# Optimization experiments

Hardware: AMD Instinct MI355X
Metric: run time of the kernel (lower is better)

## Reference

```python
import jax, jax.numpy as jnp
import numpy as np

B, N, D = 16, 2048, 128
NEG = jnp.float32(-2.0**32 + 1)

def setup_inputs() -> dict:
    key = jax.random.key(0)
    ks = jax.random.split(key, 9)
    s = 1.0 / np.sqrt(D)
    return {
        "queries": jax.random.normal(ks[0], (B, N, D), jnp.float32),
        "keys": jax.random.normal(ks[1], (B, N, D), jnp.float32),
        "padding_mask": jax.random.randint(ks[2], (B, N), 0, 2, jnp.int32),
        "Wq": jax.random.uniform(ks[3], (D, D), jnp.float32, -s, s),
        "bq": jax.random.uniform(ks[4], (D,), jnp.float32, -s, s),
        "Wk": jax.random.uniform(ks[5], (D, D), jnp.float32, -s, s),
        "bk": jax.random.uniform(ks[6], (D,), jnp.float32, -s, s),
        "Wv": jax.random.uniform(ks[7], (D, D), jnp.float32, -s, s),
        "bv": jax.random.uniform(ks[8], (D,), jnp.float32, -s, s),
    }

def reference(queries, keys, padding_mask, Wq, bq, Wk, bk, Wv, bv):
    d = queries.shape[-1]
    eq = queries @ Wq.T + bq            # [B,N,D]
    ek = keys @ Wk.T + bk               # [B,N,D]
    ev = keys @ Wv.T + bv               # [B,N,D]
    # scaled scores [B,N,N]
    coefs = jnp.einsum('bnd,bmd->bnm', eq, ek) / jnp.sqrt(jnp.float32(d))
    # key padding: large negative where keys row sums to zero (broadcast over query axis)
    key_pad = (jnp.sum(keys, axis=-1) == 0).astype(jnp.float32) * NEG   # [B,N]
    out = jnp.where(padding_mask[:, None, :] == 0, key_pad[:, None, :], coefs)
    out = jax.nn.softmax(out, axis=2)
    # NOTE: original applies query mask along the KEY axis (unsqueeze(1)) -- kept faithfully
    q_pad = (jnp.sum(queries, axis=-1) != 0).astype(jnp.float32)        # [B,N]
    out = out * q_pad[:, None, :]
    out = jnp.einsum('bnm,bmd->bnd', out, ev)
    return out + queries
```

## Files before the change

### kernel.cpp

```cpp
#include <hip/hip_runtime.h>
#include <hip/hip_bf16.h>


#define SCALE 0.08838834764831845f

typedef __bf16 bf16x8 __attribute__((ext_vector_type(8)));
typedef __bf16 bf16x4 __attribute__((ext_vector_type(4)));
typedef short  s16x4  __attribute__((ext_vector_type(4)));
typedef float  f32x4  __attribute__((ext_vector_type(4)));

static __device__ __forceinline__ f32x4 MFMA16(bf16x4 a, bf16x4 b, f32x4 c) {
#if defined(__HIP_DEVICE_COMPILE__)
    s16x4 sa, sb;
    __builtin_memcpy(&sa, &a, 8);
    __builtin_memcpy(&sb, &b, 8);
    return __builtin_amdgcn_mfma_f32_16x16x16bf16_1k(sa, sb, c, 0, 0, 0);
#else
    (void)a; (void)b;
    return c;
#endif
}

static __device__ __forceinline__ bf16x4 lo4(uint4 v) {
    bf16x4 r; uint2 t = {v.x, v.y}; __builtin_memcpy(&r, &t, 8); return r;
}
static __device__ __forceinline__ bf16x4 hi4(uint4 v) {
    bf16x4 r; uint2 t = {v.z, v.w}; __builtin_memcpy(&r, &t, 8); return r;
}

__global__ __launch_bounds__(256) void prep_kernel(
    const float* __restrict__ Wq, const float* __restrict__ Wk,
    const float* __restrict__ Wv, __bf16* __restrict__ wb)
{
    int i = blockIdx.x * 256 + threadIdx.x;
    int w = i >> 11, c = i & 2047;
    int col = c & 15, quad = (c >> 4) & 3, f = (c >> 6) & 3, ct = c >> 8;
    const float* src = ((w == 0) ? Wq : (w == 1) ? Wk : Wv)
                       + (size_t)(ct * 16 + col) * 128 + f * 32 + quad * 8;
    float4 a = *(const float4*)src, b = *(const float4*)(src + 4);
    bf16x8 t = {(__bf16)a.x, (__bf16)a.y, (__bf16)a.z, (__bf16)a.w,
                (__bf16)b.x, (__bf16)b.y, (__bf16)b.z, (__bf16)b.w};
    *(bf16x8*)&wb[(size_t)w * 16384 + (size_t)c * 8] = t;
}

__global__ __launch_bounds__(256) void proj_kernel(
    const float* __restrict__ Q, const float* __restrict__ K,
    const int* __restrict__ PM, const __bf16* __restrict__ wb,
    const float* __restrict__ Bq, const float* __restrict__ Bk,
    const float* __restrict__ Bv,
    __bf16* __restrict__ eqb, __bf16* __restrict__ ekf, __bf16* __restrict__ evf,
    float* __restrict__ dmul)
{
    __shared__ __bf16 stage[128 * 72];
    const int tid  = threadIdx.x;
    const int wave = tid >> 6, lane = tid & 63;
    const int col  = lane & 15, quad = lane >> 4;
    const int w = blockIdx.x >> 9;
    const int rowbase = (blockIdx.x & 511) * 64;
    const int myrow   = rowbase + wave * 16 + col;
    const int bb   = rowbase >> 11;
    const int m16b = (rowbase & 2047) >> 4;

    const float* asrc = (w == 0) ? Q : K;
    bf16x8 a[4];
    float ss = 0.f;
    #pragma unroll
    for (int f = 0; f < 4; ++f) {
        const float* p = asrc + (size_t)myrow * 128 + f * 32 + quad * 8;
        float4 v0 = *(const float4*)p, v1 = *(const float4*)(p + 4);
        float vv[8] = {v0.x, v0.y, v0.z, v0.w, v1.x, v1.y, v1.z, v1.w};
        #pragma unroll
        for (int j = 0; j < 8; ++j) { ss += vv[j]; a[f][j] = (__bf16)vv[j]; }
    }

    float rm = 1.f;
    if (w == 1) {
        ss += __shfl_xor(ss, 16); ss += __shfl_xor(ss, 32);
        int pmv = PM[myrow];
        rm = (pmv != 0) ? 1.f : 0.f;
        if (quad == 0) dmul[myrow] = (pmv == 0 && ss == 0.f) ? 0.f : 1.f;
    } else if (w == 2) {
        float qs = 0.f;
        #pragma unroll
        for (int f = 0; f < 4; ++f) {
            const float* p = Q + (size_t)myrow * 128 + f * 32 + quad * 8;
            float4 v0 = *(const float4*)p, v1 = *(const float4*)(p + 4);
            qs += v0.x + v0.y + v0.z + v0.w + v1.x + v1.y + v1.z + v1.w;
        }
        qs += __shfl_xor(qs, 16); qs += __shfl_xor(qs, 32);
        rm = (qs != 0.f) ? 1.f : 0.f;
    }
    float rmul[4];
    #pragma unroll
    for (int r = 0; r < 4; ++r) rmul[r] = __shfl(rm, quad * 4 + r);

    const float sc = (w == 0) ? SCALE : 1.f;
    const float* bias = (w == 0) ? Bq : (w == 1) ? Bk : Bv;
    const __bf16* wbp = wb + w * 16384;

    f32x4 acc[8];
    #pragma unroll
    for (int ct = 0; ct < 8; ++ct) { f32x4 z = {0.f, 0.f, 0.f, 0.f}; acc[ct] = z; }
    #pragma unroll
    for (int f = 0; f < 4; ++f) {
        #pragma unroll
        for (int ct = 0; ct < 8; ++ct) {
            bf16x8 bfr = *(const bf16x8*)&wbp[(size_t)(ct * 4 + f) * 512 + lane * 8];
            acc[ct] = __builtin_amdgcn_mfma_f32_16x16x32_bf16(a[f], bfr, acc[ct], 0, 0, 0);
        }
    }
    #pragma unroll
    for (int ct = 0; ct < 8; ++ct) {
        float bv = bias[ct * 16 + col];
        #pragma unroll
        for (int r = 0; r < 4; ++r) {
            float v = (acc[ct][r] + bv) * rmul[r] * sc;
            int rr = wave * 16 + quad * 4 + r;
            if (w == 2) stage[(ct * 16 + col) * 72 + rr] = (__bf16)v;
            else        stage[rr * 136 + ct * 16 + col] = (__bf16)v;
        }
    }
    __syncthreads();

    if (w == 0) {
        int r = tid >> 2, seg = (tid & 3) * 32;
        uint4* g4 = (uint4*)(eqb + (size_t)(rowbase + r) * 128 + seg);
        const uint4* s4 = (const uint4*)&stage[r * 136 + seg];
        g4[0] = s4[0]; g4[1] = s4[1]; g4[2] = s4[2]; g4[3] = s4[3];
    } else if (w == 1) {
        __bf16* dst = ekf + (size_t)bb * 2048 * 128 + (size_t)m16b * 2048;
        #pragma unroll
        for (int c = 0; c < 4; ++c) {
            int s = tid + c * 256;
            int l = s & 63, f = (s >> 6) & 3, m = s >> 8;
            *(uint4*)&dst[(size_t)s * 8] =
                *(const uint4*)&stage[(m * 16 + (l & 15)) * 136 + f * 32 + ((l >> 4) & 3) * 8];
        }
    } else {
        __bf16* dst = evf + (size_t)bb * 2048 * 128 + (size_t)m16b * 2048;
        #pragma unroll
        for (int c = 0; c < 4; ++c) {
            int s = tid + c * 256;
            int l = s & 63, dp = (s >> 6) & 3, m = s >> 8;
            int cl = l & 15, ql = (l >> 4) & 3;
            uint2 xa = *(const uint2*)&stage[((2 * dp) * 16 + cl) * 72 + m * 16 + ql * 4];
            uint2 xb = *(const uint2*)&stage[((2 * dp + 1) * 16 + cl) * 72 + m * 16 + ql * 4];
            uint4 v = {xa.x, xa.y, xb.x, xb.y};
            *(uint4*)&dst[(size_t)s * 8] = v;
        }
    }
}

__global__ __launch_bounds__(256, 2) void attn_kernel(
    const __bf16* __restrict__ eqb, const __bf16* __restrict__ ekf,
    const __bf16* __restrict__ evf, const float* __restrict__ dmul,
    const float* __restrict__ Q, float* __restrict__ out)
{
    __shared__ struct { float obuf[2][32 * 132]; float lbuf[2][32]; } sm;

    const int tid  = threadIdx.x;
    const int wave = tid >> 6, lane = tid & 63;
    const int col  = lane & 15, quad = lane >> 4;
    const int i  = blockIdx.x;
    const int b  = 2 * (i & 7) + ((i >> 3) & 1);
    const int qt = i >> 4;
    const int rowg0 = b * 2048 + qt * 32;
    const __bf16* ekb_b = ekf + (size_t)b * 2048 * 128;
    const __bf16* evb_b = evf + (size_t)b * 2048 * 128;
    const float*  dmb   = dmul + b * 2048;

    bf16x8 aqf[2][4];
    #pragma unroll
    for (int q2 = 0; q2 < 2; ++q2)
        #pragma unroll
        for (int f = 0; f < 4; ++f)
            aqf[q2][f] = *(const bf16x8*)&eqb[(size_t)(rowg0 + q2 * 16 + col) * 128 + f * 32 + quad * 8];

    f32x4 o[2][8];
    float lsum[2] = {0.f, 0.f};
    #pragma unroll
    for (int q2 = 0; q2 < 2; ++q2)
        #pragma unroll
        for (int dt = 0; dt < 8; ++dt) { f32x4 z = {0.f, 0.f, 0.f, 0.f}; o[q2][dt] = z; }

    const int kq0 = wave * 512;

    bf16x8 kc[8];
    {
        const int m16 = kq0 >> 4;
        #pragma unroll
        for (int f = 0; f < 4; ++f) {
            kc[f]     = *(const bf16x8*)&ekb_b[(size_t)((m16 + 0) * 4 + f) * 512 + lane * 8];
            kc[4 + f] = *(const bf16x8*)&ekb_b[(size_t)((m16 + 1) * 4 + f) * 512 + lane * 8];
        }
    }
    float4 dm0 = *(const float4*)&dmb[kq0 + quad * 4];
    float4 dm1 = *(const float4*)&dmb[kq0 + 16 + quad * 4];

    for (int it = 0; it < 16; ++it) {
        const int kb = kq0 + it * 32;
        const int m16 = kb >> 4;

        uint4 vc[8];
        #pragma unroll
        for (int dp = 0; dp < 4; ++dp) {
            vc[dp]     = *(const uint4*)&evb_b[(size_t)((m16 + 0) * 4 + dp) * 512 + lane * 8];
            vc[4 + dp] = *(const uint4*)&evb_b[(size_t)((m16 + 1) * 4 + dp) * 512 + lane * 8];
        }
        bf16x8 kn[8];
        float4 dn0, dn1;
        if (it < 15) {
            const int m16n = m16 + 2;
            #pragma unroll
            for (int f = 0; f < 4; ++f) {
                kn[f]     = *(const bf16x8*)&ekb_b[(size_t)((m16n + 0) * 4 + f) * 512 + lane * 8];
                kn[4 + f] = *(const bf16x8*)&ekb_b[(size_t)((m16n + 1) * 4 + f) * 512 + lane * 8];
            }
            dn0 = *(const float4*)&dmb[kb + 32 + quad * 4];
            dn1 = *(const float4*)&dmb[kb + 48 + quad * 4];
        }

        f32x4 s[2][2];
        #pragma unroll
        for (int q2 = 0; q2 < 2; ++q2)
            #pragma unroll
            for (int mt = 0; mt < 2; ++mt) { f32x4 z = {0.f, 0.f, 0.f, 0.f}; s[q2][mt] = z; }
        #pragma unroll
        for (int f = 0; f < 4; ++f) {
            #pragma unroll
            for (int q2 = 0; q2 < 2; ++q2) {
                s[q2][0] = __builtin_amdgcn_mfma_f32_16x16x32_bf16(kc[f],     aqf[q2][f], s[q2][0], 0, 0, 0);
                s[q2][1] = __builtin_amdgcn_mfma_f32_16x16x32_bf16(kc[4 + f], aqf[q2][f], s[q2][1], 0, 0, 0);
            }
        }

        const float dmv[2][4] = {{dm0.x, dm0.y, dm0.z, dm0.w},
                                 {dm1.x, dm1.y, dm1.z, dm1.w}};
        bf16x4 pk[2][2];
        #pragma unroll
        for (int q2 = 0; q2 < 2; ++q2)
            #pragma unroll
            for (int mt = 0; mt < 2; ++mt)
                #pragma unroll
                for (int r = 0; r < 4; ++r) {
                    float e = __expf(s[q2][mt][r]) * dmv[mt][r];
                    pk[q2][mt][r] = (__bf16)e;
                    lsum[q2] += e;
                }

        #pragma unroll
        for (int dp = 0; dp < 4; ++dp) {
            bf16x4 v0l = lo4(vc[dp]),     v0h = hi4(vc[dp]);
            bf16x4 v1l = lo4(vc[4 + dp]), v1h = hi4(vc[4 + dp]);
            #pragma unroll
            for (int q2 = 0; q2 < 2; ++q2) {
                o[q2][2 * dp]     = MFMA16(v0l, pk[q2][0], o[q2][2 * dp]);
                o[q2][2 * dp]     = MFMA16(v1l, pk[q2][1], o[q2][2 * dp]);
                o[q2][2 * dp + 1] = MFMA16(v0h, pk[q2][0], o[q2][2 * dp + 1]);
                o[q2][2 * dp + 1] = MFMA16(v1h, pk[q2][1], o[q2][2 * dp + 1]);
            }
        }

        if (it < 15) {
            #pragma unroll
            for (int f = 0; f < 8; ++f) kc[f] = kn[f];
            dm0 = dn0; dm1 = dn1;
        }
    }

    #pragma unroll
    for (int q2 = 0; q2 < 2; ++q2) {
        lsum[q2] += __shfl_xor(lsum[q2], 16);
        lsum[q2] += __shfl_xor(lsum[q2], 32);
    }

    if (wave & 1) {
        int slot = wave >> 1;
        #pragma unroll
        for (int q2 = 0; q2 < 2; ++q2) {
            #pragma unroll
            for (int dt = 0; dt < 8; ++dt) {
                float4 v = {o[q2][dt][0], o[q2][dt][1], o[q2][dt][2], o[q2][dt][3]};
                *(float4*)&sm.obuf[slot][(q2 * 16 + col) * 132 + dt * 16 + quad * 4] = v;
            }
            if (quad == 0) sm.lbuf[slot][q2 * 16 + col] = lsum[q2];
        }
    }
    __syncthreads();
    if (!(wave & 1)) {
        int slot = wave >> 1;
        #pragma unroll
        for (int q2 = 0; q2 < 2; ++q2) {
            lsum[q2] += sm.lbuf[slot][q2 * 16 + col];
            #pragma unroll
            for (int dt = 0; dt < 8; ++dt) {
                float4 t = *(const float4*)&sm.obuf[slot][(q2 * 16 + col) * 132 + dt * 16 + quad * 4];
                o[q2][dt][0] += t.x; o[q2][dt][1] += t.y;
                o[q2][dt][2] += t.z; o[q2][dt][3] += t.w;
            }
        }
    }
    __syncthreads();
    if (wave == 2) {
        #pragma unroll
        for (int q2 = 0; q2 < 2; ++q2) {
            #pragma unroll
            for (int dt = 0; dt < 8; ++dt) {
                float4 v = {o[q2][dt][0], o[q2][dt][1], o[q2][dt][2], o[q2][dt][3]};
                *(float4*)&sm.obuf[0][(q2 * 16 + col) * 132 + dt * 16 + quad * 4] = v;
            }
            if (quad == 0) sm.lbuf[0][q2 * 16 + col] = lsum[q2];
        }
    }
    __syncthreads();
    if (wave == 0) {
        #pragma unroll
        for (int q2 = 0; q2 < 2; ++q2) {
            float inv = 1.f / (lsum[q2] + sm.lbuf[0][q2 * 16 + col]);
            const size_t rowoff = (size_t)(rowg0 + q2 * 16 + col) * 128;
            #pragma unroll
            for (int dt = 0; dt < 8; ++dt) {
                float4 t = *(const float4*)&sm.obuf[0][(q2 * 16 + col) * 132 + dt * 16 + quad * 4];
                float4 qres = *(const float4*)&Q[rowoff + dt * 16 + quad * 4];
                float4 v;
                v.x = (o[q2][dt][0] + t.x) * inv + qres.x;
                v.y = (o[q2][dt][1] + t.y) * inv + qres.y;
                v.z = (o[q2][dt][2] + t.z) * inv + qres.z;
                v.w = (o[q2][dt][3] + t.w) * inv + qres.w;
                *(float4*)&out[rowoff + dt * 16 + quad * 4] = v;
            }
        }
    }
}

extern "C" void kernel_launch(void* const* d_in, const int* in_sizes, int n_in,
                              void* d_out, int out_size, void* d_ws, size_t ws_size,
                              hipStream_t stream)
{
    const float* Q  = (const float*)d_in[0];
    const float* K  = (const float*)d_in[1];
    const int*   PM = (const int*)d_in[2];
    const float* Wq = (const float*)d_in[3];
    const float* Bq = (const float*)d_in[4];
    const float* Wk = (const float*)d_in[5];
    const float* Bk = (const float*)d_in[6];
    const float* Wv = (const float*)d_in[7];
    const float* Bv = (const float*)d_in[8];
    float* out = (float*)d_out;

    const size_t SZE = (size_t)16 * 2048 * 128;
    __bf16* eqb = (__bf16*)d_ws;
    __bf16* ekf = eqb + SZE;
    __bf16* evf = ekf + SZE;
    float* dmul = (float*)(evf + SZE);
    __bf16* wb  = (__bf16*)(dmul + 16 * 2048);

    prep_kernel<<<24, 256, 0, stream>>>(Wq, Wk, Wv, wb);
    proj_kernel<<<1536, 256, 0, stream>>>(Q, K, PM, wb, Bq, Bk, Bv,
                                          eqb, ekf, evf, dmul);
    attn_kernel<<<1024, 256, 0, stream>>>(eqb, ekf, evf, dmul, Q, out);
}
```

Measured before the change: 160.8 us.

## Stage K/V tiles in LDS with async loads and drop cross-wave reduction

The attention kernel now uses 2-wave blocks in which each wave owns 32 query rows and walks all keys. K/V tiles are double-buffered into LDS with global_load_lds, which replaces the per-wave register prefetch from global memory and the split-key reduction through shared memory at the end. The key mask becomes an additive bias fed in as the MFMA accumulator init, instead of a multiply after exp. The projection kernel computes K and V in the same block so the key rows are loaded once, and the query-pad flags are precomputed in the prep kernel. The changes trade more per-iteration barriers and a smaller block for less redundant global traffic; the -1e5 bias only approximates the reference's -2^32 mask value.

```diff
diff --git a/kernel.cpp b/kernel.cpp
--- a/kernel.cpp
+++ b/kernel.cpp
@@ -28,28 +28,55 @@
     bf16x4 r; uint2 t = {v.z, v.w}; __builtin_memcpy(&r, &t, 8); return r;
 }
 
+static __device__ __forceinline__ void gl16(const __bf16* g, __bf16* l) {
+    __builtin_amdgcn_global_load_lds(
+        (const __attribute__((address_space(1))) unsigned int*)g,
+        (__attribute__((address_space(3))) unsigned int*)l, 16, 0, 0);
+}
+
 __global__ __launch_bounds__(256) void prep_kernel(
     const float* __restrict__ Wq, const float* __restrict__ Wk,
-    const float* __restrict__ Wv, __bf16* __restrict__ wb)
+    const float* __restrict__ Wv, const float* __restrict__ Qm,
+    __bf16* __restrict__ wb, float* __restrict__ qpadf)
 {
-    int i = blockIdx.x * 256 + threadIdx.x;
-    int w = i >> 11, c = i & 2047;
-    int col = c & 15, quad = (c >> 4) & 3, f = (c >> 6) & 3, ct = c >> 8;
-    const float* src = ((w == 0) ? Wq : (w == 1) ? Wk : Wv)
-                       + (size_t)(ct * 16 + col) * 128 + f * 32 + quad * 8;
-    float4 a = *(const float4*)src, b = *(const float4*)(src + 4);
-    bf16x8 t = {(__bf16)a.x, (__bf16)a.y, (__bf16)a.z, (__bf16)a.w,
-                (__bf16)b.x, (__bf16)b.y, (__bf16)b.z, (__bf16)b.w};
-    *(bf16x8*)&wb[(size_t)w * 16384 + (size_t)c * 8] = t;
+    if (blockIdx.x < 24) {
+        int i = blockIdx.x * 256 + threadIdx.x;
+        int w = i >> 11, c = i & 2047;
+        int col = c & 15, quad = (c >> 4) & 3, f = (c >> 6) & 3, ct = c >> 8;
+        const float* src = ((w == 0) ? Wq : (w == 1) ? Wk : Wv)
+                           + (size_t)(ct * 16 + col) * 128 + f * 32 + quad * 8;
+        float4 a = *(const float4*)src, b = *(const float4*)(src + 4);
+        bf16x8 t = {(__bf16)a.x, (__bf16)a.y, (__bf16)a.z, (__bf16)a.w,
+                    (__bf16)b.x, (__bf16)b.y, (__bf16)b.z, (__bf16)b.w};
+        *(bf16x8*)&wb[(size_t)w * 16384 + (size_t)c * 8] = t;
+    } else {
+        const int tid = threadIdx.x, wv = tid >> 6, l = tid & 63;
+        const int rb = (blockIdx.x - 24) * 256 + wv * 64;
+        #pragma unroll
+        for (int pass = 0; pass < 8; ++pass) {
+            int r = rb + pass * 8 + (l >> 3);
+            const float* p = Qm + (size_t)r * 128 + (l & 7) * 4;
+            float s4 = 0.f;
+            #pragma unroll
+            for (int seg = 0; seg < 4; ++seg) {
+                float4 v = *(const float4*)(p + seg * 32);
+                s4 += v.x + v.y + v.z + v.w;
+            }
+            s4 += __shfl_xor(s4, 1);
+            s4 += __shfl_xor(s4, 2);
+            s4 += __shfl_xor(s4, 4);
+            if ((l & 7) == 0) qpadf[r] = (s4 != 0.f) ? 1.f : 0.f;
+        }
+    }
 }
 
 __global__ __launch_bounds__(256) void proj_kernel(
     const float* __restrict__ Q, const float* __restrict__ K,
     const int* __restrict__ PM, const __bf16* __restrict__ wb,
     const float* __restrict__ Bq, const float* __restrict__ Bk,
-    const float* __restrict__ Bv,
+    const float* __restrict__ Bv, const float* __restrict__ qpadf,
     __bf16* __restrict__ eqb, __bf16* __restrict__ ekf, __bf16* __restrict__ evf,
-    float* __restrict__ dmul)
+    float* __restrict__ madd)
 {
     __shared__ __bf16 stage[128 * 72];
     const int tid  = threadIdx.x;
@@ -73,90 +100,115 @@
         for (int j = 0; j < 8; ++j) { ss += vv[j]; a[f][j] = (__bf16)vv[j]; }
     }
 
-    float rm = 1.f;
-    if (w == 1) {
-        ss += __shfl_xor(ss, 16); ss += __shfl_xor(ss, 32);
-        int pmv = PM[myrow];
-        rm = (pmv != 0) ? 1.f : 0.f;
-        if (quad == 0) dmul[myrow] = (pmv == 0 && ss == 0.f) ? 0.f : 1.f;
-    } else if (w == 2) {
-        float qs = 0.f;
+    if (w == 0) {
+        f32x4 acc[8];
+        #pragma unroll
+        for (int ct = 0; ct < 8; ++ct) { f32x4 z = {0.f, 0.f, 0.f, 0.f}; acc[ct] = z; }
         #pragma unroll
         for (int f = 0; f < 4; ++f) {
-            const float* p = Q + (size_t)myrow * 128 + f * 32 + quad * 8;
-            float4 v0 = *(const float4*)p, v1 = *(const float4*)(p + 4);
-            qs += v0.x + v0.y + v0.z + v0.w + v1.x + v1.y + v1.z + v1.w;
-        }
-        qs += __shfl_xor(qs, 16); qs += __shfl_xor(qs, 32);
-        rm = (qs != 0.f) ? 1.f : 0.f;
-    }
-    float rmul[4];
-    #pragma unroll
-    for (int r = 0; r < 4; ++r) rmul[r] = __shfl(rm, quad * 4 + r);
-
-    const float sc = (w == 0) ? SCALE : 1.f;
-    const float* bias = (w == 0) ? Bq : (w == 1) ? Bk : Bv;
-    const __bf16* wbp = wb + w * 16384;
-
-    f32x4 acc[8];
-    #pragma unroll
-    for (int ct = 0; ct < 8; ++ct) { f32x4 z = {0.f, 0.f, 0.f, 0.f}; acc[ct] = z; }
-    #pragma unroll
-    for (int f = 0; f < 4; ++f) {
+            #pragma unroll
+            for (int ct = 0; ct < 8; ++ct) {
+                bf16x8 bfr = *(const bf16x8*)&wb[(size_t)(ct * 4 + f) * 512 + lane * 8];
+                acc[ct] = __builtin_amdgcn_mfma_f32_16x16x32_bf16(a[f], bfr, acc[ct], 0, 0, 0);
+            }
+        }
         #pragma unroll
         for (int ct = 0; ct < 8; ++ct) {
-            bf16x8 bfr = *(const bf16x8*)&wbp[(size_t)(ct * 4 + f) * 512 + lane * 8];
-            acc[ct] = __builtin_amdgcn_mfma_f32_16x16x32_bf16(a[f], bfr, acc[ct], 0, 0, 0);
-        }
-    }
-    #pragma unroll
-    for (int ct = 0; ct < 8; ++ct) {
-        float bv = bias[ct * 16 + col];
-        #pragma unroll
-        for (int r = 0; r < 4; ++r) {
-            float v = (acc[ct][r] + bv) * rmul[r] * sc;
-            int rr = wave * 16 + quad * 4 + r;
-            if (w == 2) stage[(ct * 16 + col) * 72 + rr] = (__bf16)v;
-            else        stage[rr * 136 + ct * 16 + col] = (__bf16)v;
-        }
-    }
-    __syncthreads();
-
-    if (w == 0) {
+            float bvv = Bq[ct * 16 + col];
+            #pragma unroll
+            for (int r = 0; r < 4; ++r) {
+                int rr = wave * 16 + quad * 4 + r;
+                stage[rr * 136 + ct * 16 + col] = (__bf16)((acc[ct][r] + bvv) * SCALE);
+            }
+        }
+        __syncthreads();
         int r = tid >> 2, seg = (tid & 3) * 32;
         uint4* g4 = (uint4*)(eqb + (size_t)(rowbase + r) * 128 + seg);
         const uint4* s4 = (const uint4*)&stage[r * 136 + seg];
         g4[0] = s4[0]; g4[1] = s4[1]; g4[2] = s4[2]; g4[3] = s4[3];
-    } else if (w == 1) {
-        __bf16* dst = ekf + (size_t)bb * 2048 * 128 + (size_t)m16b * 2048;
-        #pragma unroll
-        for (int c = 0; c < 4; ++c) {
-            int s = tid + c * 256;
-            int l = s & 63, f = (s >> 6) & 3, m = s >> 8;
-            *(uint4*)&dst[(size_t)s * 8] =
-                *(const uint4*)&stage[(m * 16 + (l & 15)) * 136 + f * 32 + ((l >> 4) & 3) * 8];
-        }
     } else {
-        __bf16* dst = evf + (size_t)bb * 2048 * 128 + (size_t)m16b * 2048;
-        #pragma unroll
-        for (int c = 0; c < 4; ++c) {
-            int s = tid + c * 256;
-            int l = s & 63, dp = (s >> 6) & 3, m = s >> 8;
-            int cl = l & 15, ql = (l >> 4) & 3;
-            uint2 xa = *(const uint2*)&stage[((2 * dp) * 16 + cl) * 72 + m * 16 + ql * 4];
-            uint2 xb = *(const uint2*)&stage[((2 * dp + 1) * 16 + cl) * 72 + m * 16 + ql * 4];
-            uint4 v = {xa.x, xa.y, xb.x, xb.y};
-            *(uint4*)&dst[(size_t)s * 8] = v;
-        }
-    }
-}
-
-__global__ __launch_bounds__(256, 2) void attn_kernel(
+        ss += __shfl_xor(ss, 16); ss += __shfl_xor(ss, 32);
+        int pmv = PM[myrow];
+        float rmk = (pmv != 0) ? 1.f : 0.f;
+        float rmv = qpadf[myrow];
+        if (quad == 0) madd[myrow] = (pmv == 0 && ss == 0.f) ? -1.0e5f : 0.f;
+        float rk[4], rv[4];
+        #pragma unroll
+        for (int r = 0; r < 4; ++r) {
+            rk[r] = __shfl(rmk, quad * 4 + r);
+            rv[r] = __shfl(rmv, quad * 4 + r);
+        }
+
+        f32x4 acck[8], accv[8];
+        #pragma unroll
+        for (int ct = 0; ct < 8; ++ct) {
+            f32x4 z = {0.f, 0.f, 0.f, 0.f}; acck[ct] = z; accv[ct] = z;
+        }
+        #pragma unroll
+        for (int f = 0; f < 4; ++f) {
+            #pragma unroll
+            for (int ct = 0; ct < 8; ++ct) {
+                bf16x8 bk_ = *(const bf16x8*)&wb[(size_t)16384 + (size_t)(ct * 4 + f) * 512 + lane * 8];
+                bf16x8 bv_ = *(const bf16x8*)&wb[(size_t)32768 + (size_t)(ct * 4 + f) * 512 + lane * 8];
+                acck[ct] = __builtin_amdgcn_mfma_f32_16x16x32_bf16(a[f], bk_, acck[ct], 0, 0, 0);
+                accv[ct] = __builtin_amdgcn_mfma_f32_16x16x32_bf16(a[f], bv_, accv[ct], 0, 0, 0);
+            }
+        }
+
+        #pragma unroll
+        for (int ct = 0; ct < 8; ++ct) {
+            float bvv = Bk[ct * 16 + col];
+            #pragma unroll
+            for (int r = 0; r < 4; ++r) {
+                int rr = wave * 16 + quad * 4 + r;
+                stage[rr * 136 + ct * 16 + col] = (__bf16)((acck[ct][r] + bvv) * rk[r]);
+            }
+        }
+        __syncthreads();
+        {
+            __bf16* dst = ekf + (size_t)bb * 2048 * 128 + (size_t)m16b * 2048;
+            #pragma unroll
+            for (int c = 0; c < 4; ++c) {
+                int s = tid + c * 256;
+                int l = s & 63, f = (s >> 6) & 3, m = s >> 8;
+                *(uint4*)&dst[(size_t)s * 8] =
+                    *(const uint4*)&stage[(m * 16 + (l & 15)) * 136 + f * 32 + ((l >> 4) & 3) * 8];
+            }
+        }
+        __syncthreads();
+        #pragma unroll
+        for (int ct = 0; ct < 8; ++ct) {
+            float bvv = Bv[ct * 16 + col];
+            #pragma unroll
+            for (int r = 0; r < 4; ++r) {
+                int rr = wave * 16 + quad * 4 + r;
+                stage[(ct * 16 + col) * 72 + rr] = (__bf16)((accv[ct][r] + bvv) * rv[r]);
+            }
+        }
+        __syncthreads();
+        {
+            __bf16* dst = evf + (size_t)bb * 2048 * 128 + (size_t)m16b * 2048;
+            #pragma unroll
+            for (int c = 0; c < 4; ++c) {
+                int s = tid + c * 256;
+                int l = s & 63, dp = (s >> 6) & 3, m = s >> 8;
+                int cl = l & 15, ql = (l >> 4) & 3;
+                uint2 xa = *(const uint2*)&stage[((2 * dp) * 16 + cl) * 72 + m * 16 + ql * 4];
+                uint2 xb = *(const uint2*)&stage[((2 * dp + 1) * 16 + cl) * 72 + m * 16 + ql * 4];
+                uint4 v = {xa.x, xa.y, xb.x, xb.y};
+                *(uint4*)&dst[(size_t)s * 8] = v;
+            }
+        }
+    }
+}
+
+__global__ __launch_bounds__(128) void attn_kernel(
     const __bf16* __restrict__ eqb, const __bf16* __restrict__ ekf,
-    const __bf16* __restrict__ evf, const float* __restrict__ dmul,
+    const __bf16* __restrict__ evf, const float* __restrict__ madd,
     const float* __restrict__ Q, float* __restrict__ out)
 {
-    __shared__ struct { float obuf[2][32 * 132]; float lbuf[2][32]; } sm;
+    __shared__ __bf16 kb[2][4096];
+    __shared__ __bf16 vb[2][4096];
 
     const int tid  = threadIdx.x;
     const int wave = tid >> 6, lane = tid & 63;
@@ -164,10 +216,10 @@
     const int i  = blockIdx.x;
     const int b  = 2 * (i & 7) + ((i >> 3) & 1);
     const int qt = i >> 4;
-    const int rowg0 = b * 2048 + qt * 32;
+    const int rowg0 = b * 2048 + qt * 64 + wave * 32;
     const __bf16* ekb_b = ekf + (size_t)b * 2048 * 128;
     const __bf16* evb_b = evf + (size_t)b * 2048 * 128;
-    const float*  dmb   = dmul + b * 2048;
+    const float*  dmb   = madd + b * 2048;
 
     bf16x8 aqf[2][4];
     #pragma unroll
@@ -183,48 +235,51 @@
         #pragma unroll
         for (int dt = 0; dt < 8; ++dt) { f32x4 z = {0.f, 0.f, 0.f, 0.f}; o[q2][dt] = z; }
 
-    const int kq0 = wave * 512;
-
-    bf16x8 kc[8];
-    {
-        const int m16 = kq0 >> 4;
+    #pragma unroll
+    for (int c = 0; c < 4; ++c) {
+        int sb = (c * 2 + wave) * 64;
+        gl16(ekb_b + (size_t)(sb + lane) * 8, &kb[0][sb * 8]);
+        gl16(evb_b + (size_t)(sb + lane) * 8, &vb[0][sb * 8]);
+    }
+    float4 dm0 = *(const float4*)&dmb[quad * 4];
+    float4 dm1 = *(const float4*)&dmb[16 + quad * 4];
+    __syncthreads();
+
+    for (int t = 0; t < 64; ++t) {
+        const int cur = t & 1;
+        float4 dn0, dn1;
+        if (t < 63) {
+            const __bf16* gk = ekb_b + (size_t)(t + 1) * 4096;
+            const __bf16* gv = evb_b + (size_t)(t + 1) * 4096;
+            #pragma unroll
+            for (int c = 0; c < 4; ++c) {
+                int sb = (c * 2 + wave) * 64;
+                gl16(gk + (size_t)(sb + lane) * 8, &kb[cur ^ 1][sb * 8]);
+                gl16(gv + (size_t)(sb + lane) * 8, &vb[cur ^ 1][sb * 8]);
+            }
+            dn0 = *(const float4*)&dmb[(t + 1) * 32 + quad * 4];
+            dn1 = *(const float4*)&dmb[(t + 1) * 32 + 16 + quad * 4];
+        }
+
+        bf16x8 kc[8];
+        uint4  vc[8];
         #pragma unroll
         for (int f = 0; f < 4; ++f) {
-            kc[f]     = *(const bf16x8*)&ekb_b[(size_t)((m16 + 0) * 4 + f) * 512 + lane * 8];
-            kc[4 + f] = *(const bf16x8*)&ekb_b[(size_t)((m16 + 1) * 4 + f) * 512 + lane * 8];
-        }
-    }
-    float4 dm0 = *(const float4*)&dmb[kq0 + quad * 4];
-    float4 dm1 = *(const float4*)&dmb[kq0 + 16 + quad * 4];
-
-    for (int it = 0; it < 16; ++it) {
-        const int kb = kq0 + it * 32;
-        const int m16 = kb >> 4;
-
-        uint4 vc[8];
+            kc[f]     = *(const bf16x8*)&kb[cur][f * 512 + lane * 8];
+            kc[4 + f] = *(const bf16x8*)&kb[cur][(4 + f) * 512 + lane * 8];
+        }
         #pragma unroll
         for (int dp = 0; dp < 4; ++dp) {
-            vc[dp]     = *(const uint4*)&evb_b[(size_t)((m16 + 0) * 4 + dp) * 512 + lane * 8];
-            vc[4 + dp] = *(const uint4*)&evb_b[(size_t)((m16 + 1) * 4 + dp) * 512 + lane * 8];
-        }
-        bf16x8 kn[8];
-        float4 dn0, dn1;
-        if (it < 15) {
-            const int m16n = m16 + 2;
-            #pragma unroll
-            for (int f = 0; f < 4; ++f) {
-                kn[f]     = *(const bf16x8*)&ekb_b[(size_t)((m16n + 0) * 4 + f) * 512 + lane * 8];
-                kn[4 + f] = *(const bf16x8*)&ekb_b[(size_t)((m16n + 1) * 4 + f) * 512 + lane * 8];
-            }
-            dn0 = *(const float4*)&dmb[kb + 32 + quad * 4];
-            dn1 = *(const float4*)&dmb[kb + 48 + quad * 4];
+            vc[dp]     = *(const uint4*)&vb[cur][dp * 512 + lane * 8];
+            vc[4 + dp] = *(const uint4*)&vb[cur][(4 + dp) * 512 + lane * 8];
         }
 
         f32x4 s[2][2];
-        #pragma unroll
-        for (int q2 = 0; q2 < 2; ++q2)
-            #pragma unroll
-            for (int mt = 0; mt < 2; ++mt) { f32x4 z = {0.f, 0.f, 0.f, 0.f}; s[q2][mt] = z; }
+        {
+            f32x4 i0 = {dm0.x, dm0.y, dm0.z, dm0.w};
+            f32x4 i1 = {dm1.x, dm1.y, dm1.z, dm1.w};
+            s[0][0] = i0; s[0][1] = i1; s[1][0] = i0; s[1][1] = i1;
+        }
         #pragma unroll
         for (int f = 0; f < 4; ++f) {
             #pragma unroll
@@ -234,8 +289,6 @@
             }
         }
 
-        const float dmv[2][4] = {{dm0.x, dm0.y, dm0.z, dm0.w},
-                                 {dm1.x, dm1.y, dm1.z, dm1.w}};
         bf16x4 pk[2][2];
         #pragma unroll
         for (int q2 = 0; q2 < 2; ++q2)
@@ -243,7 +296,7 @@
             for (int mt = 0; mt < 2; ++mt)
                 #pragma unroll
                 for (int r = 0; r < 4; ++r) {
-                    float e = __expf(s[q2][mt][r]) * dmv[mt][r];
+                    float e = __expf(s[q2][mt][r]);
                     pk[q2][mt][r] = (__bf16)e;
                     lsum[q2] += e;
                 }
@@ -261,10 +314,9 @@
             }
         }
 
-        if (it < 15) {
-            #pragma unroll
-            for (int f = 0; f < 8; ++f) kc[f] = kn[f];
+        if (t < 63) {
             dm0 = dn0; dm1 = dn1;
+            __syncthreads();
         }
     }
 
@@ -272,63 +324,17 @@
     for (int q2 = 0; q2 < 2; ++q2) {
         lsum[q2] += __shfl_xor(lsum[q2], 16);
         lsum[q2] += __shfl_xor(lsum[q2], 32);
-    }
-
-    if (wave & 1) {
-        int slot = wave >> 1;
-        #pragma unroll
-        for (int q2 = 0; q2 < 2; ++q2) {
-            #pragma unroll
-            for (int dt = 0; dt < 8; ++dt) {
-                float4 v = {o[q2][dt][0], o[q2][dt][1], o[q2][dt][2], o[q2][dt][3]};
-                *(float4*)&sm.obuf[slot][(q2 * 16 + col) * 132 + dt * 16 + quad * 4] = v;
-            }
-            if (quad == 0) sm.lbuf[slot][q2 * 16 + col] = lsum[q2];
-        }
-    }
-    __syncthreads();
-    if (!(wave & 1)) {
-        int slot = wave >> 1;
-        #pragma unroll
-        for (int q2 = 0; q2 < 2; ++q2) {
-            lsum[q2] += sm.lbuf[slot][q2 * 16 + col];
-            #pragma unroll
-            for (int dt = 0; dt < 8; ++dt) {
-                float4 t = *(const float4*)&sm.obuf[slot][(q2 * 16 + col) * 132 + dt * 16 + quad * 4];
-                o[q2][dt][0] += t.x; o[q2][dt][1] += t.y;
-                o[q2][dt][2] += t.z; o[q2][dt][3] += t.w;
-            }
-        }
-    }
-    __syncthreads();
-    if (wave == 2) {
-        #pragma unroll
-        for (int q2 = 0; q2 < 2; ++q2) {
-            #pragma unroll
-            for (int dt = 0; dt < 8; ++dt) {
-                float4 v = {o[q2][dt][0], o[q2][dt][1], o[q2][dt][2], o[q2][dt][3]};
-                *(float4*)&sm.obuf[0][(q2 * 16 + col) * 132 + dt * 16 + quad * 4] = v;
-            }
-            if (quad == 0) sm.lbuf[0][q2 * 16 + col] = lsum[q2];
-        }
-    }
-    __syncthreads();
-    if (wave == 0) {
-        #pragma unroll
-        for (int q2 = 0; q2 < 2; ++q2) {
-            float inv = 1.f / (lsum[q2] + sm.lbuf[0][q2 * 16 + col]);
-            const size_t rowoff = (size_t)(rowg0 + q2 * 16 + col) * 128;
-            #pragma unroll
-            for (int dt = 0; dt < 8; ++dt) {
-                float4 t = *(const float4*)&sm.obuf[0][(q2 * 16 + col) * 132 + dt * 16 + quad * 4];
-                float4 qres = *(const float4*)&Q[rowoff + dt * 16 + quad * 4];
-                float4 v;
-                v.x = (o[q2][dt][0] + t.x) * inv + qres.x;
-                v.y = (o[q2][dt][1] + t.y) * inv + qres.y;
-                v.z = (o[q2][dt][2] + t.z) * inv + qres.z;
-                v.w = (o[q2][dt][3] + t.w) * inv + qres.w;
-                *(float4*)&out[rowoff + dt * 16 + quad * 4] = v;
-            }
+        float inv = 1.f / lsum[q2];
+        const size_t rowoff = (size_t)(rowg0 + q2 * 16 + col) * 128;
+        #pragma unroll
+        for (int dt = 0; dt < 8; ++dt) {
+            float4 qres = *(const float4*)&Q[rowoff + dt * 16 + quad * 4];
+            float4 v;
+            v.x = o[q2][dt][0] * inv + qres.x;
+            v.y = o[q2][dt][1] * inv + qres.y;
+            v.z = o[q2][dt][2] * inv + qres.z;
+            v.w = o[q2][dt][3] * inv + qres.w;
+            *(float4*)&out[rowoff + dt * 16 + quad * 4] = v;
         }
     }
 }
@@ -352,11 +358,12 @@
     __bf16* eqb = (__bf16*)d_ws;
     __bf16* ekf = eqb + SZE;
     __bf16* evf = ekf + SZE;
-    float* dmul = (float*)(evf + SZE);
-    __bf16* wb  = (__bf16*)(dmul + 16 * 2048);
-
-    prep_kernel<<<24, 256, 0, stream>>>(Wq, Wk, Wv, wb);
-    proj_kernel<<<1536, 256, 0, stream>>>(Q, K, PM, wb, Bq, Bk, Bv,
-                                          eqb, ekf, evf, dmul);
-    attn_kernel<<<1024, 256, 0, stream>>>(eqb, ekf, evf, dmul, Q, out);
-}
+    float* madd = (float*)(evf + SZE);
+    __bf16* wb  = (__bf16*)(madd + 16 * 2048);
+    float* qpadf = (float*)(wb + 3 * 16384);
+
+    prep_kernel<<<152, 256, 0, stream>>>(Wq, Wk, Wv, Q, wb, qpadf);
+    proj_kernel<<<1024, 256, 0, stream>>>(Q, K, PM, wb, Bq, Bk, Bv, qpadf,
+                                          eqb, ekf, evf, madd);
+    attn_kernel<<<512, 128, 0, stream>>>(eqb, ekf, evf, madd, Q, out);
+}
```

Result: slower. 218.7 us (+36.0%).

## Use K=32 MFMA for PV, fold log2e scale and additive mask into scores

Applied to the files above, without the earlier changes.

Rearranges the value tensor layout so the P·V product uses the 16x16x32 bf16 MFMA instead of pairs of 16x16x16 MFMAs. It folds log2(e) into the query scale so the kernel can use the hardware exp2. The multiplicative key mask becomes an additive bias that seeds the score accumulator. It also adds s_setprio around the MFMA blocks and pads the reduction buffer stride. The aim is fewer MFMA issues and less VALU work per iteration. The risk is that the -1e5 additive mask and the exp without max subtraction approximate the original zeroing semantics.

```diff
diff --git a/kernel.cpp b/kernel.cpp
--- a/kernel.cpp
+++ b/kernel.cpp
@@ -2,30 +2,17 @@
 #include <hip/hip_bf16.h>
 
 
-#define SCALE 0.08838834764831845f
+#define SCALE_LOG2E 0.12751875f
 
 typedef __bf16 bf16x8 __attribute__((ext_vector_type(8)));
-typedef __bf16 bf16x4 __attribute__((ext_vector_type(4)));
-typedef short  s16x4  __attribute__((ext_vector_type(4)));
 typedef float  f32x4  __attribute__((ext_vector_type(4)));
 
-static __device__ __forceinline__ f32x4 MFMA16(bf16x4 a, bf16x4 b, f32x4 c) {
-#if defined(__HIP_DEVICE_COMPILE__)
-    s16x4 sa, sb;
-    __builtin_memcpy(&sa, &a, 8);
-    __builtin_memcpy(&sb, &b, 8);
-    return __builtin_amdgcn_mfma_f32_16x16x16bf16_1k(sa, sb, c, 0, 0, 0);
+static __device__ __forceinline__ float fexp2(float x) {
+#if __has_builtin(__builtin_amdgcn_exp2f)
+    return __builtin_amdgcn_exp2f(x);
 #else
-    (void)a; (void)b;
-    return c;
+    float r; asm("v_exp_f32 %0, %1" : "=v"(r) : "v"(x)); return r;
 #endif
-}
-
-static __device__ __forceinline__ bf16x4 lo4(uint4 v) {
-    bf16x4 r; uint2 t = {v.x, v.y}; __builtin_memcpy(&r, &t, 8); return r;
-}
-static __device__ __forceinline__ bf16x4 hi4(uint4 v) {
-    bf16x4 r; uint2 t = {v.z, v.w}; __builtin_memcpy(&r, &t, 8); return r;
 }
 
 __global__ __launch_bounds__(256) void prep_kernel(
@@ -49,7 +36,7 @@
     const float* __restrict__ Bq, const float* __restrict__ Bk,
     const float* __restrict__ Bv,
     __bf16* __restrict__ eqb, __bf16* __restrict__ ekf, __bf16* __restrict__ evf,
-    float* __restrict__ dmul)
+    float* __restrict__ madd)
 {
     __shared__ __bf16 stage[128 * 72];
     const int tid  = threadIdx.x;
@@ -78,7 +65,7 @@
         ss += __shfl_xor(ss, 16); ss += __shfl_xor(ss, 32);
         int pmv = PM[myrow];
         rm = (pmv != 0) ? 1.f : 0.f;
-        if (quad == 0) dmul[myrow] = (pmv == 0 && ss == 0.f) ? 0.f : 1.f;
+        if (quad == 0) madd[myrow] = (pmv == 0 && ss == 0.f) ? -1.0e5f : 0.f;
     } else if (w == 2) {
         float qs = 0.f;
         #pragma unroll
@@ -94,7 +81,7 @@
     #pragma unroll
     for (int r = 0; r < 4; ++r) rmul[r] = __shfl(rm, quad * 4 + r);
 
-    const float sc = (w == 0) ? SCALE : 1.f;
+    const float sc = (w == 0) ? SCALE_LOG2E : 1.f;
     const float* bias = (w == 0) ? Bq : (w == 1) ? Bk : Bv;
     const __bf16* wbp = wb + w * 16384;
 
@@ -137,14 +124,14 @@
                 *(const uint4*)&stage[(m * 16 + (l & 15)) * 136 + f * 32 + ((l >> 4) & 3) * 8];
         }
     } else {
-        __bf16* dst = evf + (size_t)bb * 2048 * 128 + (size_t)m16b * 2048;
+        __bf16* dst = evf + (size_t)bb * 2048 * 128 + (size_t)(rowbase & 2047) * 128;
         #pragma unroll
         for (int c = 0; c < 4; ++c) {
             int s = tid + c * 256;
-            int l = s & 63, dp = (s >> 6) & 3, m = s >> 8;
-            int cl = l & 15, ql = (l >> 4) & 3;
-            uint2 xa = *(const uint2*)&stage[((2 * dp) * 16 + cl) * 72 + m * 16 + ql * 4];
-            uint2 xb = *(const uint2*)&stage[((2 * dp + 1) * 16 + cl) * 72 + m * 16 + ql * 4];
+            int l = s & 63, dt = (s >> 6) & 7, tl = s >> 9;
+            int cl = l & 15, ql = l >> 4;
+            uint2 xa = *(const uint2*)&stage[(dt * 16 + cl) * 72 + tl * 32 + ql * 4];
+            uint2 xb = *(const uint2*)&stage[(dt * 16 + cl) * 72 + tl * 32 + 16 + ql * 4];
             uint4 v = {xa.x, xa.y, xb.x, xb.y};
             *(uint4*)&dst[(size_t)s * 8] = v;
         }
@@ -153,10 +140,10 @@
 
 __global__ __launch_bounds__(256, 2) void attn_kernel(
     const __bf16* __restrict__ eqb, const __bf16* __restrict__ ekf,
-    const __bf16* __restrict__ evf, const float* __restrict__ dmul,
+    const __bf16* __restrict__ evf, const float* __restrict__ madd,
     const float* __restrict__ Q, float* __restrict__ out)
 {
-    __shared__ struct { float obuf[2][32 * 132]; float lbuf[2][32]; } sm;
+    __shared__ struct { float obuf[2][32 * 140]; float lbuf[2][32]; } sm;
 
     const int tid  = threadIdx.x;
     const int wave = tid >> 6, lane = tid & 63;
@@ -167,7 +154,7 @@
     const int rowg0 = b * 2048 + qt * 32;
     const __bf16* ekb_b = ekf + (size_t)b * 2048 * 128;
     const __bf16* evb_b = evf + (size_t)b * 2048 * 128;
-    const float*  dmb   = dmul + b * 2048;
+    const float*  dmb   = madd + b * 2048;
 
     bf16x8 aqf[2][4];
     #pragma unroll
@@ -199,18 +186,17 @@
 
     for (int it = 0; it < 16; ++it) {
         const int kb = kq0 + it * 32;
-        const int m16 = kb >> 4;
-
-        uint4 vc[8];
-        #pragma unroll
-        for (int dp = 0; dp < 4; ++dp) {
-            vc[dp]     = *(const uint4*)&evb_b[(size_t)((m16 + 0) * 4 + dp) * 512 + lane * 8];
-            vc[4 + dp] = *(const uint4*)&evb_b[(size_t)((m16 + 1) * 4 + dp) * 512 + lane * 8];
-        }
+        const int t32 = kb >> 5;
+
+        bf16x8 vf[8];
+        #pragma unroll
+        for (int dt = 0; dt < 8; ++dt)
+            vf[dt] = *(const bf16x8*)&evb_b[((size_t)t32 * 8 + dt) * 512 + lane * 8];
+
         bf16x8 kn[8];
         float4 dn0, dn1;
         if (it < 15) {
-            const int m16n = m16 + 2;
+            const int m16n = (kb >> 4) + 2;
             #pragma unroll
             for (int f = 0; f < 4; ++f) {
                 kn[f]     = *(const bf16x8*)&ekb_b[(size_t)((m16n + 0) * 4 + f) * 512 + lane * 8];
@@ -221,10 +207,12 @@
         }
 
         f32x4 s[2][2];
-        #pragma unroll
-        for (int q2 = 0; q2 < 2; ++q2)
-            #pragma unroll
-            for (int mt = 0; mt < 2; ++mt) { f32x4 z = {0.f, 0.f, 0.f, 0.f}; s[q2][mt] = z; }
+        {
+            f32x4 i0 = {dm0.x, dm0.y, dm0.z, dm0.w};
+            f32x4 i1 = {dm1.x, dm1.y, dm1.z, dm1.w};
+            s[0][0] = i0; s[0][1] = i1; s[1][0] = i0; s[1][1] = i1;
+        }
+        __builtin_amdgcn_s_setprio(1);
         #pragma unroll
         for (int f = 0; f < 4; ++f) {
             #pragma unroll
@@ -233,33 +221,28 @@
                 s[q2][1] = __builtin_amdgcn_mfma_f32_16x16x32_bf16(kc[4 + f], aqf[q2][f], s[q2][1], 0, 0, 0);
             }
         }
-
-        const float dmv[2][4] = {{dm0.x, dm0.y, dm0.z, dm0.w},
-                                 {dm1.x, dm1.y, dm1.z, dm1.w}};
-        bf16x4 pk[2][2];
+        __builtin_amdgcn_s_setprio(0);
+
+        bf16x8 pq[2];
         #pragma unroll
         for (int q2 = 0; q2 < 2; ++q2)
             #pragma unroll
-            for (int mt = 0; mt < 2; ++mt)
+            for (int g = 0; g < 2; ++g)
                 #pragma unroll
                 for (int r = 0; r < 4; ++r) {
-                    float e = __expf(s[q2][mt][r]) * dmv[mt][r];
-                    pk[q2][mt][r] = (__bf16)e;
+                    float e = fexp2(s[q2][g][r]);
+                    pq[q2][g * 4 + r] = (__bf16)e;
                     lsum[q2] += e;
                 }
 
-        #pragma unroll
-        for (int dp = 0; dp < 4; ++dp) {
-            bf16x4 v0l = lo4(vc[dp]),     v0h = hi4(vc[dp]);
-            bf16x4 v1l = lo4(vc[4 + dp]), v1h = hi4(vc[4 + dp]);
-            #pragma unroll
-            for (int q2 = 0; q2 < 2; ++q2) {
-                o[q2][2 * dp]     = MFMA16(v0l, pk[q2][0], o[q2][2 * dp]);
-                o[q2][2 * dp]     = MFMA16(v1l, pk[q2][1], o[q2][2 * dp]);
-                o[q2][2 * dp + 1] = MFMA16(v0h, pk[q2][0], o[q2][2 * dp + 1]);
-                o[q2][2 * dp + 1] = MFMA16(v1h, pk[q2][1], o[q2][2 * dp + 1]);
-            }
-        }
+        __builtin_amdgcn_s_setprio(1);
+        #pragma unroll
+        for (int dt = 0; dt < 8; ++dt) {
+            #pragma unroll
+            for (int q2 = 0; q2 < 2; ++q2)
+                o[q2][dt] = __builtin_amdgcn_mfma_f32_16x16x32_bf16(vf[dt], pq[q2], o[q2][dt], 0, 0, 0);
+        }
+        __builtin_amdgcn_s_setprio(0);
 
         if (it < 15) {
             #pragma unroll
@@ -281,7 +264,7 @@
             #pragma unroll
             for (int dt = 0; dt < 8; ++dt) {
                 float4 v = {o[q2][dt][0], o[q2][dt][1], o[q2][dt][2], o[q2][dt][3]};
-                *(float4*)&sm.obuf[slot][(q2 * 16 + col) * 132 + dt * 16 + quad * 4] = v;
+                *(float4*)&sm.obuf[slot][(q2 * 16 + col) * 140 + dt * 16 + quad * 4] = v;
             }
             if (quad == 0) sm.lbuf[slot][q2 * 16 + col] = lsum[q2];
         }
@@ -294,7 +277,7 @@
             lsum[q2] += sm.lbuf[slot][q2 * 16 + col];
             #pragma unroll
             for (int dt = 0; dt < 8; ++dt) {
-                float4 t = *(const float4*)&sm.obuf[slot][(q2 * 16 + col) * 132 + dt * 16 + quad * 4];
+                float4 t = *(const float4*)&sm.obuf[slot][(q2 * 16 + col) * 140 + dt * 16 + quad * 4];
                 o[q2][dt][0] += t.x; o[q2][dt][1] += t.y;
                 o[q2][dt][2] += t.z; o[q2][dt][3] += t.w;
             }
@@ -307,7 +290,7 @@
             #pragma unroll
             for (int dt = 0; dt < 8; ++dt) {
                 float4 v = {o[q2][dt][0], o[q2][dt][1], o[q2][dt][2], o[q2][dt][3]};
-                *(float4*)&sm.obuf[0][(q2 * 16 + col) * 132 + dt * 16 + quad * 4] = v;
+                *(float4*)&sm.obuf[0][(q2 * 16 + col) * 140 + dt * 16 + quad * 4] = v;
             }
             if (quad == 0) sm.lbuf[0][q2 * 16 + col] = lsum[q2];
         }
@@ -320,7 +303,7 @@
             const size_t rowoff = (size_t)(rowg0 + q2 * 16 + col) * 128;
             #pragma unroll
             for (int dt = 0; dt < 8; ++dt) {
-                float4 t = *(const float4*)&sm.obuf[0][(q2 * 16 + col) * 132 + dt * 16 + quad * 4];
+                float4 t = *(const float4*)&sm.obuf[0][(q2 * 16 + col) * 140 + dt * 16 + quad * 4];
                 float4 qres = *(const float4*)&Q[rowoff + dt * 16 + quad * 4];
                 float4 v;
                 v.x = (o[q2][dt][0] + t.x) * inv + qres.x;
@@ -352,11 +335,11 @@
     __bf16* eqb = (__bf16*)d_ws;
     __bf16* ekf = eqb + SZE;
     __bf16* evf = ekf + SZE;
-    float* dmul = (float*)(evf + SZE);
-    __bf16* wb  = (__bf16*)(dmul + 16 * 2048);
+    float* madd = (float*)(evf + SZE);
+    __bf16* wb  = (__bf16*)(madd + 16 * 2048);
 
     prep_kernel<<<24, 256, 0, stream>>>(Wq, Wk, Wv, wb);
     proj_kernel<<<1536, 256, 0, stream>>>(Q, K, PM, wb, Bq, Bk, Bv,
-                                          eqb, ekf, evf, dmul);
-    attn_kernel<<<1024, 256, 0, stream>>>(eqb, ekf, evf, dmul, Q, out);
-}
+                                          eqb, ekf, evf, madd);
+    attn_kernel<<<1024, 256, 0, stream>>>(eqb, ekf, evf, madd, Q, out);
+}
```

Result: no change. 161.7 us (+0.6%).
